# Kernel tuning notes

Hardware: AMD Instinct MI355X
Metric: run time of the kernel (lower is better)

## Reference

```python
import jax, jax.numpy as jnp
import numpy as np


def setup_inputs() -> dict:
    key = jax.random.key(0)
    kq, kk, kv = jax.random.split(key, 3)
    B, H, N, D = 4, 8, 2048, 64
    q = jax.random.normal(kq, (B, H, N, D), dtype=jnp.float32)
    k = jax.random.normal(kk, (B, H, N, D), dtype=jnp.float32)
    v = jax.random.normal(kv, (B, H, N, D), dtype=jnp.float32)
    return {"q": q, "k": k, "v": v}


def reference(q, k, v):
    # Naive attention exactly as the torch module: full [B,H,N,N] scores.
    scale = q.shape[-1] ** -0.5
    sim = jnp.einsum('bhid,bhjd->bhij', q, k) * scale  # [B,H,N,N]
    attn = jax.nn.softmax(sim, axis=-1)
    # dropout p=0.0 -> identity (module default; eval mode)
    out = jnp.einsum('bhij,bhjd->bhid', attn, v)  # [B,H,N,D]
    return out
```

## Files before the change

kernel.cpp:

```cpp
#include <hip/hip_runtime.h>

#define NN   2048
#define DD   64
#define NTW  8
#define BH   32
#define BHND (BH * NN * DD)
#define SC   0.18033688f
#define TSH  8192

typedef float    f32x4  __attribute__((ext_vector_type(4)));
typedef short    bf16x8 __attribute__((ext_vector_type(8)));
typedef unsigned u32x4  __attribute__((ext_vector_type(4)));

#define WAIT_VM0()   asm volatile("s_waitcnt vmcnt(0)" ::: "memory")
#define SFENCE()     __builtin_amdgcn_sched_barrier(0)
#define SBAR()       __builtin_amdgcn_s_barrier()

__device__ __forceinline__ short f2bf(float x){
    unsigned u = __float_as_uint(x);
    u += 0x7FFF + ((u >> 16) & 1);
    return (short)(u >> 16);
}

__device__ __forceinline__ unsigned cvt_pk(float lo, float hi){
    unsigned r;
    asm("v_cvt_pk_bf16_f32 %0, %1, %2" : "=v"(r) : "v"(lo), "v"(hi));
    return r;
}

__device__ __forceinline__ float exp2_fast(float x){
    float r;
    asm("v_exp_f32 %0, %1" : "=v"(r) : "v"(x));
    return r;
}

__device__ __forceinline__ void gload_lds16(const short* g, short* l) {
    __builtin_amdgcn_global_load_lds(
        (const __attribute__((address_space(1))) void*)g,
        (__attribute__((address_space(3))) void*)l, 16, 0, 0);
}

__global__ __launch_bounds__(256)
void prep_frag(const float* __restrict__ k, const float* __restrict__ v,
               short* __restrict__ fr)
{
    const int tile = blockIdx.x;
    const int bh   = blockIdx.y;
    const int tid  = threadIdx.x;
    const int lane = tid & 63;
    const int f    = tid >> 6;
    const int l16  = lane & 15;
    const int lg   = lane >> 4;
    const long base = (long)bh * NN * DD;
    const int  kv0  = tile * 64;
    short* tb = fr + ((long)bh * 32 + tile) * TSH;

    {
        const float* src = k + base + (long)(kv0 + f * 16 + l16) * DD + lg * 8;
        #pragma unroll
        for (int c = 0; c < 2; ++c) {
            f32x4 x0 = *(const f32x4*)(src + c * 32);
            f32x4 x1 = *(const f32x4*)(src + c * 32 + 4);
            bf16x8 o;
            #pragma unroll
            for (int j = 0; j < 4; ++j) { o[j] = f2bf(x0[j]); o[4 + j] = f2bf(x1[j]); }
            *(bf16x8*)(tb + ((f * 2 + c) * 64 + lane) * 8) = o;
        }
    }
    {
        const float* vb = v + base;
        #pragma unroll
        for (int kk = 0; kk < 2; ++kk) {
            bf16x8 o;
            #pragma unroll
            for (int i = 0; i < 8; ++i) {
                float x = vb[(long)(kv0 + kk * 32 + (i >> 2) * 16 + lg * 4 + (i & 3)) * DD
                             + f * 16 + l16];
                o[i] = f2bf(x);
            }
            *(bf16x8*)(tb + ((8 + f * 2 + kk) * 64 + lane) * 8) = o;
        }
    }
}

__global__ __launch_bounds__(256, 2)
void attn_fwd_v25(const float* __restrict__ q,
                  const short* __restrict__ fr,
                  float* __restrict__ out)
{
    const int l     = blockIdx.x;
    const int xcd   = l & 7;
    const int idx   = l >> 3;
    const int qtile = idx & 15;
    const int bh    = xcd + 8 * (idx >> 4);

    const int tid   = threadIdx.x;
    const int wave  = tid >> 6;
    const int qg    = wave & 1;
    const int kvh   = wave >> 1;
    const int lane  = tid & 63;
    const int l16   = lane & 15;
    const int lg    = lane >> 4;

    __shared__ __align__(16) short k_lds[2][2][8192];

    const long base  = (long)bh * NN * DD;
    const int  qrow0 = qtile * 128 + qg * 64;

    bf16x8 aq[4][2];
    #pragma unroll
    for (int j = 0; j < 4; ++j) {
        const float* qp = q + base + (long)(qrow0 + j * 16 + l16) * DD + lg * 8;
        #pragma unroll
        for (int c = 0; c < 2; ++c) {
            f32x4 x0 = *(const f32x4*)(qp + c * 32);
            f32x4 x1 = *(const f32x4*)(qp + c * 32 + 4);
            u32x4 pk;
            pk[0] = cvt_pk(x0[0] * SC, x0[1] * SC);
            pk[1] = cvt_pk(x0[2] * SC, x0[3] * SC);
            pk[2] = cvt_pk(x1[0] * SC, x1[1] * SC);
            pk[3] = cvt_pk(x1[2] * SC, x1[3] * SC);
            aq[j][c] = __builtin_bit_cast(bf16x8, pk);
        }
    }

    bf16x8 ones;
    #pragma unroll
    for (int ii = 0; ii < 8; ++ii) ones[ii] = (short)0x3F80;

    const short* fbase = fr + ((long)bh * 32 + kvh * 16) * TSH + lane * 8;

    auto stageK = [&](int buf, int tt) {
        const short* s0 = fbase + (long)(2 * tt) * TSH + qg * 4 * 512;
        const short* s1 = fbase + (long)(2 * tt + 1) * TSH + qg * 4 * 512;
        short* d0 = &k_lds[kvh][buf][qg * 4 * 512];
        short* d1 = &k_lds[kvh][buf][4096 + qg * 4 * 512];
        #pragma unroll
        for (int j = 0; j < 4; ++j) gload_lds16(s0 + j * 512, d0 + j * 512);
        #pragma unroll
        for (int j = 0; j < 4; ++j) gload_lds16(s1 + j * 512, d1 + j * 512);
    };

    f32x4 acc[4][4];
    f32x4 accS[4];
    #pragma unroll
    for (int t = 0; t < 4; ++t)
        #pragma unroll
        for (int j = 0; j < 4; ++j) acc[t][j] = f32x4{0.f, 0.f, 0.f, 0.f};
    #pragma unroll
    for (int j = 0; j < 4; ++j) accS[j] = f32x4{0.f, 0.f, 0.f, 0.f};

    stageK(0, 0);

    #pragma unroll 1
    for (int t = 0; t < NTW; ++t) {
        WAIT_VM0(); SFENCE();
        SBAR(); SFENCE();
        if (t + 1 < NTW) stageK((t + 1) & 1, t + 1);

        #pragma unroll
        for (int u = 0; u < 2; ++u) {
            const short* lb   = &k_lds[kvh][t & 1][u * 4096 + lane * 8];
            const short* vsrc = fbase + (long)(2 * t + u) * TSH;

            #pragma unroll
            for (int kk = 0; kk < 2; ++kk) {
                bf16x8 bvv[4];
                #pragma unroll
                for (int t2 = 0; t2 < 4; ++t2)
                    bvv[t2] = *(const bf16x8*)(vsrc + (8 + t2 * 2 + kk) * 512);

                bf16x8 ka[2][2];
                #pragma unroll
                for (int cb = 0; cb < 2; ++cb)
                    #pragma unroll
                    for (int c = 0; c < 2; ++c)
                        ka[cb][c] = *(const bf16x8*)(lb + (((2 * kk + cb) * 2 + c)) * 512);

                f32x4 s[2][4];
                __builtin_amdgcn_s_setprio(1);
                #pragma unroll
                for (int cb = 0; cb < 2; ++cb)
                    #pragma unroll
                    for (int j = 0; j < 4; ++j) {
                        f32x4 z = f32x4{0.f, 0.f, 0.f, 0.f};
                        z = __builtin_amdgcn_mfma_f32_16x16x32_bf16(ka[cb][0], aq[j][0], z, 0, 0, 0);
                        z = __builtin_amdgcn_mfma_f32_16x16x32_bf16(ka[cb][1], aq[j][1], z, 0, 0, 0);
                        s[cb][j] = z;
                    }
                __builtin_amdgcn_s_setprio(0);

                bf16x8 pa[4];
                #pragma unroll
                for (int j = 0; j < 4; ++j) {
                    #pragma unroll
                    for (int cb = 0; cb < 2; ++cb)
                        #pragma unroll
                        for (int r = 0; r < 4; ++r)
                            s[cb][j][r] = exp2_fast(s[cb][j][r]);
                    u32x4 w;
                    w[0] = cvt_pk(s[0][j][0], s[0][j][1]);
                    w[1] = cvt_pk(s[0][j][2], s[0][j][3]);
                    w[2] = cvt_pk(s[1][j][0], s[1][j][1]);
                    w[3] = cvt_pk(s[1][j][2], s[1][j][3]);
                    pa[j] = __builtin_bit_cast(bf16x8, w);
                }

                __builtin_amdgcn_s_setprio(1);
                #pragma unroll
                for (int t2 = 0; t2 < 4; ++t2)
                    #pragma unroll
                    for (int j = 0; j < 4; ++j)
                        acc[t2][j] = __builtin_amdgcn_mfma_f32_16x16x32_bf16(pa[j], bvv[t2], acc[t2][j], 0, 0, 0);
                #pragma unroll
                for (int j = 0; j < 4; ++j)
                    accS[j] = __builtin_amdgcn_mfma_f32_16x16x32_bf16(pa[j], ones, accS[j], 0, 0, 0);
                __builtin_amdgcn_s_setprio(0);
            }
        }
    }

    __syncthreads();

    float* slot = (float*)&k_lds[0][0][0];
    if (kvh == 1) {
        float* sp = slot + qg * 5120;
        #pragma unroll
        for (int t2 = 0; t2 < 4; ++t2)
            #pragma unroll
            for (int j = 0; j < 4; ++j)
                *(f32x4*)&sp[((t2 * 4 + j) * 64 + lane) * 4] = acc[t2][j];
        #pragma unroll
        for (int j = 0; j < 4; ++j)
            *(f32x4*)&sp[((16 + j) * 64 + lane) * 4] = accS[j];
    }
    __syncthreads();

    if (kvh == 0) {
        const float* sp = slot + qg * 5120;
        #pragma unroll
        for (int j = 0; j < 4; ++j)
            accS[j] += *(const f32x4*)&sp[((16 + j) * 64 + lane) * 4];
        float* op = out + base + (long)qrow0 * DD;
        #pragma unroll
        for (int j = 0; j < 4; ++j) {
            f32x4 inv;
            #pragma unroll
            for (int r = 0; r < 4; ++r) inv[r] = 1.f / accS[j][r];
            #pragma unroll
            for (int t2 = 0; t2 < 4; ++t2) {
                f32x4 o = acc[t2][j] + *(const f32x4*)&sp[((t2 * 4 + j) * 64 + lane) * 4];
                #pragma unroll
                for (int r = 0; r < 4; ++r)
                    op[(long)(j * 16 + lg * 4 + r) * DD + t2 * 16 + l16] = o[r] * inv[r];
            }
        }
    }
}

extern "C" void kernel_launch(void* const* d_in, const int* in_sizes, int n_in,
                              void* d_out, int out_size, void* d_ws, size_t ws_size,
                              hipStream_t stream) {
    const float* q = (const float*)d_in[0];
    const float* k = (const float*)d_in[1];
    const float* v = (const float*)d_in[2];
    float* out = (float*)d_out;

    short* fr = (short*)d_ws;
    prep_frag<<<dim3(32, BH), 256, 0, stream>>>(k, v, fr);
    attn_fwd_v25<<<512, 256, 0, stream>>>(q, fr, out);
    (void)ws_size;
}
```

Before: 51.77 us.

## Load fp32 K directly into LDS and convert in-kernel, prep only V

The prep kernel no longer converts K to bf16 fragments; the attention kernel now streams raw fp32 K tiles into LDS with async global-to-LDS loads and packs them to bf16 while reading fragments. The KV loop is restructured to 64-key tiles over 16 iterations, with V fragments loaded once per tile. The aim is to remove the K prep pass and its workspace write and read-back. In exchange the main kernel reads twice as many K bytes, does extra conversion ALU work, and runs twice as many barrier-synchronised iterations.

Result: slower. 59.88 us (+15.7%).

```diff
diff --git a/kernel.cpp b/kernel.cpp
--- a/kernel.cpp
+++ b/kernel.cpp
@@ -2,11 +2,12 @@
 
 #define NN   2048
 #define DD   64
-#define NTW  8
+#define KVB  64
+#define NTW  16
 #define BH   32
 #define BHND (BH * NN * DD)
 #define SC   0.18033688f
-#define TSH  8192
+#define VTSH 4096
 
 typedef float    f32x4  __attribute__((ext_vector_type(4)));
 typedef short    bf16x8 __attribute__((ext_vector_type(8)));
@@ -34,15 +35,14 @@
     return r;
 }
 
-__device__ __forceinline__ void gload_lds16(const short* g, short* l) {
+__device__ __forceinline__ void gload_lds16f(const float* g, float* l) {
     __builtin_amdgcn_global_load_lds(
         (const __attribute__((address_space(1))) void*)g,
         (__attribute__((address_space(3))) void*)l, 16, 0, 0);
 }
 
 __global__ __launch_bounds__(256)
-void prep_frag(const float* __restrict__ k, const float* __restrict__ v,
-               short* __restrict__ fr)
+void prep_v(const float* __restrict__ v, short* __restrict__ fr)
 {
     const int tile = blockIdx.x;
     const int bh   = blockIdx.y;
@@ -52,39 +52,26 @@
     const int l16  = lane & 15;
     const int lg   = lane >> 4;
     const long base = (long)bh * NN * DD;
-    const int  kv0  = tile * 64;
-    short* tb = fr + ((long)bh * 32 + tile) * TSH;
-
-    {
-        const float* src = k + base + (long)(kv0 + f * 16 + l16) * DD + lg * 8;
-        #pragma unroll
-        for (int c = 0; c < 2; ++c) {
-            f32x4 x0 = *(const f32x4*)(src + c * 32);
-            f32x4 x1 = *(const f32x4*)(src + c * 32 + 4);
-            bf16x8 o;
-            #pragma unroll
-            for (int j = 0; j < 4; ++j) { o[j] = f2bf(x0[j]); o[4 + j] = f2bf(x1[j]); }
-            *(bf16x8*)(tb + ((f * 2 + c) * 64 + lane) * 8) = o;
-        }
-    }
-    {
-        const float* vb = v + base;
-        #pragma unroll
-        for (int kk = 0; kk < 2; ++kk) {
-            bf16x8 o;
-            #pragma unroll
-            for (int i = 0; i < 8; ++i) {
-                float x = vb[(long)(kv0 + kk * 32 + (i >> 2) * 16 + lg * 4 + (i & 3)) * DD
-                             + f * 16 + l16];
-                o[i] = f2bf(x);
-            }
-            *(bf16x8*)(tb + ((8 + f * 2 + kk) * 64 + lane) * 8) = o;
-        }
+    const int  kv0  = tile * KVB;
+    short* tb = fr + ((long)bh * 32 + tile) * VTSH;
+
+    const float* vb = v + base;
+    #pragma unroll
+    for (int kk = 0; kk < 2; ++kk) {
+        bf16x8 o;
+        #pragma unroll
+        for (int i = 0; i < 8; ++i) {
+            float x = vb[(long)(kv0 + kk * 32 + (i >> 2) * 16 + lg * 4 + (i & 3)) * DD
+                         + f * 16 + l16];
+            o[i] = f2bf(x);
+        }
+        *(bf16x8*)(tb + ((f * 2 + kk) * 64 + lane) * 8) = o;
     }
 }
 
 __global__ __launch_bounds__(256, 2)
-void attn_fwd_v25(const float* __restrict__ q,
+void attn_fwd_v29(const float* __restrict__ q,
+                  const float* __restrict__ kf,
                   const short* __restrict__ fr,
                   float* __restrict__ out)
 {
@@ -102,7 +89,7 @@
     const int l16   = lane & 15;
     const int lg    = lane >> 4;
 
-    __shared__ __align__(16) short k_lds[2][2][8192];
+    __shared__ __align__(16) float k_lds[2][2][4096];
 
     const long base  = (long)bh * NN * DD;
     const int  qrow0 = qtile * 128 + qg * 64;
@@ -128,17 +115,20 @@
     #pragma unroll
     for (int ii = 0; ii < 8; ++ii) ones[ii] = (short)0x3F80;
 
-    const short* fbase = fr + ((long)bh * 32 + kvh * 16) * TSH + lane * 8;
+    const float* kbase = kf + base;
+    const short* vbase = fr + ((long)bh * 32 + kvh * NTW) * VTSH + lane * 8;
 
     auto stageK = [&](int buf, int tt) {
-        const short* s0 = fbase + (long)(2 * tt) * TSH + qg * 4 * 512;
-        const short* s1 = fbase + (long)(2 * tt + 1) * TSH + qg * 4 * 512;
-        short* d0 = &k_lds[kvh][buf][qg * 4 * 512];
-        short* d1 = &k_lds[kvh][buf][4096 + qg * 4 * 512];
-        #pragma unroll
-        for (int j = 0; j < 4; ++j) gload_lds16(s0 + j * 512, d0 + j * 512);
-        #pragma unroll
-        for (int j = 0; j < 4; ++j) gload_lds16(s1 + j * 512, d1 + j * 512);
+        const int kv0 = kvh * (NN / 2) + tt * KVB;
+        #pragma unroll
+        for (int fi = 0; fi < 4; ++fi) {
+            const int f = qg * 4 + fi;
+            const float* src = kbase + (long)(kv0 + (f >> 1) * 16 + l16) * DD
+                               + (f & 1) * 32 + lg * 8;
+            #pragma unroll
+            for (int h = 0; h < 2; ++h)
+                gload_lds16f(src + h * 4, &k_lds[kvh][buf][f * 512 + h * 256]);
+        }
     };
 
     f32x4 acc[4][4];
@@ -158,65 +148,73 @@
         SBAR(); SFENCE();
         if (t + 1 < NTW) stageK((t + 1) & 1, t + 1);
 
-        #pragma unroll
-        for (int u = 0; u < 2; ++u) {
-            const short* lb   = &k_lds[kvh][t & 1][u * 4096 + lane * 8];
-            const short* vsrc = fbase + (long)(2 * t + u) * TSH;
-
-            #pragma unroll
-            for (int kk = 0; kk < 2; ++kk) {
-                bf16x8 bvv[4];
-                #pragma unroll
-                for (int t2 = 0; t2 < 4; ++t2)
-                    bvv[t2] = *(const bf16x8*)(vsrc + (8 + t2 * 2 + kk) * 512);
-
-                bf16x8 ka[2][2];
+        const short* vsrc = vbase + (long)t * VTSH;
+        bf16x8 bvv[2][4];
+        #pragma unroll
+        for (int kk = 0; kk < 2; ++kk)
+            #pragma unroll
+            for (int t2 = 0; t2 < 4; ++t2)
+                bvv[kk][t2] = *(const bf16x8*)(vsrc + (t2 * 2 + kk) * 512);
+
+        const float* lb = &k_lds[kvh][t & 1][lane * 4];
+
+        #pragma unroll
+        for (int kk = 0; kk < 2; ++kk) {
+            bf16x8 ka[2][2];
+            #pragma unroll
+            for (int cb = 0; cb < 2; ++cb)
+                #pragma unroll
+                for (int c = 0; c < 2; ++c) {
+                    const int f = (2 * kk + cb) * 2 + c;
+                    f32x4 x0 = *(const f32x4*)(lb + f * 512);
+                    f32x4 x1 = *(const f32x4*)(lb + f * 512 + 256);
+                    u32x4 pk;
+                    pk[0] = cvt_pk(x0[0], x0[1]);
+                    pk[1] = cvt_pk(x0[2], x0[3]);
+                    pk[2] = cvt_pk(x1[0], x1[1]);
+                    pk[3] = cvt_pk(x1[2], x1[3]);
+                    ka[cb][c] = __builtin_bit_cast(bf16x8, pk);
+                }
+
+            f32x4 s[2][4];
+            __builtin_amdgcn_s_setprio(1);
+            #pragma unroll
+            for (int cb = 0; cb < 2; ++cb)
+                #pragma unroll
+                for (int j = 0; j < 4; ++j) {
+                    f32x4 z = f32x4{0.f, 0.f, 0.f, 0.f};
+                    z = __builtin_amdgcn_mfma_f32_16x16x32_bf16(ka[cb][0], aq[j][0], z, 0, 0, 0);
+                    z = __builtin_amdgcn_mfma_f32_16x16x32_bf16(ka[cb][1], aq[j][1], z, 0, 0, 0);
+                    s[cb][j] = z;
+                }
+            __builtin_amdgcn_s_setprio(0);
+
+            bf16x8 pa[4];
+            #pragma unroll
+            for (int j = 0; j < 4; ++j) {
                 #pragma unroll
                 for (int cb = 0; cb < 2; ++cb)
                     #pragma unroll
-                    for (int c = 0; c < 2; ++c)
-                        ka[cb][c] = *(const bf16x8*)(lb + (((2 * kk + cb) * 2 + c)) * 512);
-
-                f32x4 s[2][4];
-                __builtin_amdgcn_s_setprio(1);
-                #pragma unroll
-                for (int cb = 0; cb < 2; ++cb)
-                    #pragma unroll
-                    for (int j = 0; j < 4; ++j) {
-                        f32x4 z = f32x4{0.f, 0.f, 0.f, 0.f};
-                        z = __builtin_amdgcn_mfma_f32_16x16x32_bf16(ka[cb][0], aq[j][0], z, 0, 0, 0);
-                        z = __builtin_amdgcn_mfma_f32_16x16x32_bf16(ka[cb][1], aq[j][1], z, 0, 0, 0);
-                        s[cb][j] = z;
-                    }
-                __builtin_amdgcn_s_setprio(0);
-
-                bf16x8 pa[4];
-                #pragma unroll
-                for (int j = 0; j < 4; ++j) {
-                    #pragma unroll
-                    for (int cb = 0; cb < 2; ++cb)
-                        #pragma unroll
-                        for (int r = 0; r < 4; ++r)
-                            s[cb][j][r] = exp2_fast(s[cb][j][r]);
-                    u32x4 w;
-                    w[0] = cvt_pk(s[0][j][0], s[0][j][1]);
-                    w[1] = cvt_pk(s[0][j][2], s[0][j][3]);
-                    w[2] = cvt_pk(s[1][j][0], s[1][j][1]);
-                    w[3] = cvt_pk(s[1][j][2], s[1][j][3]);
-                    pa[j] = __builtin_bit_cast(bf16x8, w);
-                }
-
-                __builtin_amdgcn_s_setprio(1);
-                #pragma unroll
-                for (int t2 = 0; t2 < 4; ++t2)
-                    #pragma unroll
-                    for (int j = 0; j < 4; ++j)
-                        acc[t2][j] = __builtin_amdgcn_mfma_f32_16x16x32_bf16(pa[j], bvv[t2], acc[t2][j], 0, 0, 0);
+                    for (int r = 0; r < 4; ++r)
+                        s[cb][j][r] = exp2_fast(s[cb][j][r]);
+                u32x4 w;
+                w[0] = cvt_pk(s[0][j][0], s[0][j][1]);
+                w[1] = cvt_pk(s[0][j][2], s[0][j][3]);
+                w[2] = cvt_pk(s[1][j][0], s[1][j][1]);
+                w[3] = cvt_pk(s[1][j][2], s[1][j][3]);
+                pa[j] = __builtin_bit_cast(bf16x8, w);
+            }
+
+            __builtin_amdgcn_s_setprio(1);
+            #pragma unroll
+            for (int t2 = 0; t2 < 4; ++t2)
                 #pragma unroll
                 for (int j = 0; j < 4; ++j)
-                    accS[j] = __builtin_amdgcn_mfma_f32_16x16x32_bf16(pa[j], ones, accS[j], 0, 0, 0);
-                __builtin_amdgcn_s_setprio(0);
-            }
+                    acc[t2][j] = __builtin_amdgcn_mfma_f32_16x16x32_bf16(pa[j], bvv[kk][t2], acc[t2][j], 0, 0, 0);
+            #pragma unroll
+            for (int j = 0; j < 4; ++j)
+                accS[j] = __builtin_amdgcn_mfma_f32_16x16x32_bf16(pa[j], ones, accS[j], 0, 0, 0);
+            __builtin_amdgcn_s_setprio(0);
         }
     }
 
@@ -267,7 +265,7 @@
     float* out = (float*)d_out;
 
     short* fr = (short*)d_ws;
-    prep_frag<<<dim3(32, BH), 256, 0, stream>>>(k, v, fr);
-    attn_fwd_v25<<<512, 256, 0, stream>>>(q, fr, out);
+    prep_v<<<dim3(32, BH), 256, 0, stream>>>(v, fr);
+    attn_fwd_v29<<<512, 256, 0, stream>>>(q, k, fr, out);
     (void)ws_size;
 }
```
